# Optimization experiments

Hardware: AMD Instinct MI355X
Metric: run time of the kernel (lower is better)

## Reference

```python
import jax, jax.numpy as jnp
import numpy as np

N, E = 50000, 640000          # nodes, edges
F_IN, HID, CLS = 128, 128, 64  # feature dims


def setup_inputs() -> dict:
    key = jax.random.key(0)
    ks = jax.random.split(key, 12)
    x = jax.random.normal(ks[0], (N, F_IN), dtype=jnp.float32)
    edge_index = jax.random.randint(ks[1], (2, E), 0, N, dtype=jnp.int32)
    s_in = 1.0 / np.sqrt(F_IN)
    s_h = 1.0 / np.sqrt(HID)
    return {
        "x": x,
        "edge_index": edge_index,
        "W0": jax.random.normal(ks[2], (F_IN, HID), jnp.float32) * s_in,
        "b0": jnp.zeros((HID,), jnp.float32),
        "W1": jax.random.normal(ks[3], (HID, HID), jnp.float32) * s_h,
        "b1": jnp.zeros((HID,), jnp.float32),
        "W2": jax.random.normal(ks[4], (HID, HID), jnp.float32) * s_h,
        "b2": jnp.zeros((HID,), jnp.float32),
        "W_lin": jax.random.normal(ks[5], (HID, CLS), jnp.float32) * s_h,
        "b_lin": jnp.zeros((CLS,), jnp.float32),
    }


def reference(x, edge_index, W0, b0, W1, b1, W2, b2, W_lin, b_lin):
    # GCNConv (PyG defaults): out = D^-1/2 (A + I) D^-1/2 (x @ W) + b
    row, col = edge_index[0], edge_index[1]  # source -> target
    # degree with self-loop (graph is fixed across layers, compute norms once)
    deg = jnp.zeros((N,), x.dtype).at[col].add(1.0) + 1.0
    dinv = jax.lax.rsqrt(deg)                 # deg >= 1, safe
    enorm = (dinv[row] * dinv[col])[:, None]  # [E,1] edge norm
    snorm = (dinv * dinv)[:, None]            # [N,1] self-loop norm

    def conv(h, W, b):
        h = h @ W                                             # [N,HID]
        agg = jnp.zeros_like(h).at[col].add(h[row] * enorm)   # neighbor agg
        return agg + h * snorm + b                            # + self loop + bias

    h = jax.nn.relu(conv(x, W0, b0))
    h = jax.nn.relu(conv(h, W1, b1))
    h = jax.nn.relu(conv(h, W2, b2))
    return h @ W_lin + b_lin
```

## Files before the change

### kernel.cpp

```cpp
#include <hip/hip_runtime.h>
#include <hip/hip_fp16.h>

#define N_NODES 50000
#define HID 128
#define CLS 64

#define NBINS 196
#define NBLK 256
#define LBUF_CAP 4096
#define WTOT 57344
#define GEMM0_BLOCKS 782
#define AROW 136

typedef __attribute__((ext_vector_type(8))) _Float16 f16x8;
typedef __attribute__((ext_vector_type(4))) float f32x4;

__global__ __launch_bounds__(256) void hist_wsplit_kernel(
    const int* __restrict__ col, int* __restrict__ hist,
    const float* __restrict__ W0, const float* __restrict__ W1,
    const float* __restrict__ W2, const float* __restrict__ Wl,
    __half* __restrict__ o0h, __half* __restrict__ o0l,
    __half* __restrict__ o1h, __half* __restrict__ o1l,
    __half* __restrict__ o2h, __half* __restrict__ o2l,
    __half* __restrict__ o3h, __half* __restrict__ o3l,
    int E, int chunk) {
    int widx = blockIdx.x * 256 + threadIdx.x;
    if (widx < WTOT) {
        const float* W;
        __half *oh, *ol;
        int NCdim, local;
        if (widx < 16384)      { W = W0; oh = o0h; ol = o0l; NCdim = 128; local = widx; }
        else if (widx < 32768) { W = W1; oh = o1h; ol = o1l; NCdim = 128; local = widx - 16384; }
        else if (widx < 49152) { W = W2; oh = o2h; ol = o2l; NCdim = 128; local = widx - 32768; }
        else                   { W = Wl; oh = o3h; ol = o3l; NCdim = 64;  local = widx - 49152; }
        int nn = local >> 7;
        int k = local & 127;
        float v = W[(size_t)k * NCdim + nn];
        __half h = __float2half_rn(v);
        oh[local] = h;
        ol[local] = __float2half_rn(v - __half2float(h));
    }
    __shared__ int h[NBINS];
    for (int i = threadIdx.x; i < NBINS; i += 256) h[i] = 0;
    __syncthreads();
    int b = blockIdx.x;
    int beg = b * chunk;
    int end = min(E, beg + chunk);
    if (beg < end) {
        int vend = beg + ((end - beg) & ~3);
        for (int i = beg + threadIdx.x * 4; i < vend; i += 1024) {
            int4 c4 = *(const int4*)(col + i);
            atomicAdd(&h[c4.x >> 8], 1);
            atomicAdd(&h[c4.y >> 8], 1);
            atomicAdd(&h[c4.z >> 8], 1);
            atomicAdd(&h[c4.w >> 8], 1);
        }
        int i = vend + threadIdx.x;
        if (i < end) atomicAdd(&h[col[i] >> 8], 1);
    }
    __syncthreads();
    for (int i = threadIdx.x; i < NBINS; i += 256)
        hist[i * NBLK + b] = h[i];
}

__global__ __launch_bounds__(256) void scatter_kernel(
    const int* __restrict__ row, const int* __restrict__ col,
    const int* __restrict__ hist, int* __restrict__ binBase_g,
    int* __restrict__ sbuf_src, unsigned char* __restrict__ sbuf_c,
    int E, int chunk) {
    __shared__ int sTot[256];
    __shared__ int cur[NBINS];
    int b = blockIdx.x, t = threadIdx.x;
    int partial = 0, total = 0;
    if (t < NBINS) {
        const int4* r4 = (const int4*)(hist + t * NBLK);
        int nb4 = b >> 2, rem = b & 3;
        for (int j = 0; j < NBLK / 4; ++j) {
            int4 v = r4[j];
            int s = v.x + v.y + v.z + v.w;
            total += s;
            if (j < nb4) partial += s;
            else if (j == nb4) {
                if (rem > 0) partial += v.x;
                if (rem > 1) partial += v.y;
                if (rem > 2) partial += v.z;
            }
        }
    }
    sTot[t] = (t < NBINS) ? total : 0;
    __syncthreads();
#pragma unroll
    for (int off = 1; off < 256; off <<= 1) {
        int u = (t >= off) ? sTot[t - off] : 0;
        __syncthreads();
        sTot[t] += u;
        __syncthreads();
    }
    int myBase = sTot[t] - total;
    if (t < NBINS) cur[t] = myBase + partial;
    if (b == 0) {
        if (t < NBINS) binBase_g[t] = myBase;
        if (t == 0) binBase_g[NBINS] = E;
    }
    __syncthreads();
    int beg = b * chunk;
    int end = min(E, beg + chunk);
    if (beg >= end) return;
    int vend = beg + ((end - beg) & ~3);
    for (int i = beg + t * 4; i < vend; i += 1024) {
        int4 c4 = *(const int4*)(col + i);
        int4 r4 = *(const int4*)(row + i);
        int p;
        p = atomicAdd(&cur[c4.x >> 8], 1); sbuf_src[p] = r4.x; sbuf_c[p] = (unsigned char)(c4.x & 255);
        p = atomicAdd(&cur[c4.y >> 8], 1); sbuf_src[p] = r4.y; sbuf_c[p] = (unsigned char)(c4.y & 255);
        p = atomicAdd(&cur[c4.z >> 8], 1); sbuf_src[p] = r4.z; sbuf_c[p] = (unsigned char)(c4.z & 255);
        p = atomicAdd(&cur[c4.w >> 8], 1); sbuf_src[p] = r4.w; sbuf_c[p] = (unsigned char)(c4.w & 255);
    }
    int i = vend + t;
    if (i < end) {
        int c = col[i];
        int p = atomicAdd(&cur[c >> 8], 1);
        sbuf_src[p] = row[i];
        sbuf_c[p] = (unsigned char)(c & 255);
    }
}

__device__ __forceinline__ void gemm0_body(
    const float* __restrict__ x, const __half* __restrict__ Bh,
    const __half* __restrict__ Bl, __half* __restrict__ C, int M, int rowTile) {
    constexpr int NT = 8;
    int lane = threadIdx.x & 63;
    int m0 = rowTile << 4;
    if (m0 >= M) return;
    int mr = lane & 15;
    int kq = (lane >> 4) << 3;

    const float*  af = x + (size_t)(m0 + mr) * 128 + kq;
    const __half* bh = Bh + (size_t)mr * 128 + kq;
    const __half* bl = Bl + (size_t)mr * 128 + kq;

    f32x4 acc[NT];
#pragma unroll
    for (int t = 0; t < NT; ++t) acc[t] = (f32x4){0.f, 0.f, 0.f, 0.f};
#pragma unroll
    for (int kc = 0; kc < 128; kc += 32) {
        float4 lo = *(const float4*)(af + kc);
        float4 hi = *(const float4*)(af + kc + 4);
        f16x8 a;
        a[0] = (_Float16)lo.x; a[1] = (_Float16)lo.y;
        a[2] = (_Float16)lo.z; a[3] = (_Float16)lo.w;
        a[4] = (_Float16)hi.x; a[5] = (_Float16)hi.y;
        a[6] = (_Float16)hi.z; a[7] = (_Float16)hi.w;
#pragma unroll
        for (int t = 0; t < NT; ++t) {
            f16x8 wh = *(const f16x8*)(bh + (size_t)t * 16 * 128 + kc);
            f16x8 wl = *(const f16x8*)(bl + (size_t)t * 16 * 128 + kc);
            acc[t] = __builtin_amdgcn_mfma_f32_16x16x32_f16(a, wh, acc[t], 0, 0, 0);
            acc[t] = __builtin_amdgcn_mfma_f32_16x16x32_f16(a, wl, acc[t], 0, 0, 0);
        }
    }
    int r0 = m0 + ((lane >> 4) << 2);
    int cc = lane & 15;
#pragma unroll
    for (int t = 0; t < NT; ++t)
#pragma unroll
        for (int r = 0; r < 4; ++r)
            C[(size_t)(r0 + r) * 128 + t * 16 + cc] =
                __float2half_rn(acc[t][r]);
}

__global__ __launch_bounds__(256) void csrplace_gemm0_kernel(
    const int* __restrict__ binBase,
    const int* __restrict__ sbuf_src, const unsigned char* __restrict__ sbuf_c,
    float* __restrict__ dinv, int* __restrict__ row_ptr, int* __restrict__ csr_src,
    const float* __restrict__ x, const __half* __restrict__ W0h,
    const __half* __restrict__ W0l, __half* __restrict__ h2, int n, int E) {
    __shared__ int lcnt[256];
    __shared__ int lcur[256];
    __shared__ int ss[256];
    __shared__ int lbuf[LBUF_CAP];
    int b = blockIdx.x;
    if (b >= NBINS) {
        gemm0_body(x, W0h, W0l, h2, n, (b - NBINS) * 4 + (threadIdx.x >> 6));
        return;
    }
    int t = threadIdx.x;
    lcnt[t] = 0;
    __syncthreads();
    int beg = binBase[b], end = binBase[b + 1];
    for (int j = beg + t; j < end; j += 256)
        atomicAdd(&lcnt[sbuf_c[j]], 1);
    __syncthreads();
    int deg = lcnt[t];
    int node = b * 256 + t;
    if (node < n) dinv[node] = rsqrtf((float)deg + 1.0f);
    ss[t] = deg;
    __syncthreads();
#pragma unroll
    for (int off = 1; off < 256; off <<= 1) {
        int u = (t >= off) ? ss[t - off] : 0;
        __syncthreads();
        ss[t] += u;
        __syncthreads();
    }
    int excl = ss[t] - deg;
    lcur[t] = excl;
    int total = ss[255];
    if (node < n) row_ptr[node] = beg + excl;
    if (b == 0 && t == 0) row_ptr[n] = E;
    __syncthreads();
    for (int j = beg + t; j < end; j += 256) {
        int c = sbuf_c[j];
        int pos = atomicAdd(&lcur[c], 1);
        lbuf[pos] = sbuf_src[j];
    }
    __syncthreads();
    for (int j = t; j < total; j += 256) csr_src[beg + j] = lbuf[j];
}

template<int NC, bool HEAD>
__global__ __launch_bounds__(256) void agg_gemm_kernel(
    const __half* __restrict__ h2, const int* __restrict__ row_ptr,
    const int* __restrict__ csr_src, const float* __restrict__ dinv,
    const float* __restrict__ bias,
    const __half* __restrict__ Bh, const __half* __restrict__ Bl,
    const float* __restrict__ gbias, void* __restrict__ Cv, int n) {
    __shared__ __half Als[16][AROW];
    int wave = threadIdx.x >> 6;
    int lane = threadIdx.x & 63;
    int loff = lane << 1;
    int m0 = blockIdx.x << 4;

#pragma unroll
    for (int k = 0; k < 4; ++k) {
        int lr = wave * 4 + k;
        int wid = m0 + lr;
        if (wid >= n) break;
        int beg = row_ptr[wid];
        int end = row_ptr[wid + 1];
        float dv = dinv[wid];
        float ax = 0.f, ay = 0.f;
        for (int base = beg; base < end; base += 64) {
            int cnt = end - base;
            if (cnt > 64) cnt = 64;
            int msrc = 0;
            float mw = 0.f;
            if (lane < cnt) {
                msrc = csr_src[base + lane];
                mw = dinv[msrc] * dv;
            }
            int j = 0;
            for (; j + 8 <= cnt; j += 8) {
                int s0 = __shfl(msrc, j),     s1 = __shfl(msrc, j + 1);
                int s2 = __shfl(msrc, j + 2), s3 = __shfl(msrc, j + 3);
                int s4 = __shfl(msrc, j + 4), s5 = __shfl(msrc, j + 5);
                int s6 = __shfl(msrc, j + 6), s7 = __shfl(msrc, j + 7);
                float w0 = __shfl(mw, j),     w1 = __shfl(mw, j + 1);
                float w2 = __shfl(mw, j + 2), w3 = __shfl(mw, j + 3);
                float w4 = __shfl(mw, j + 4), w5 = __shfl(mw, j + 5);
                float w6 = __shfl(mw, j + 6), w7 = __shfl(mw, j + 7);
                float2 v0 = __half22float2(*(const __half2*)(h2 + ((size_t)s0 << 7) + loff));
                float2 v1 = __half22float2(*(const __half2*)(h2 + ((size_t)s1 << 7) + loff));
                float2 v2 = __half22float2(*(const __half2*)(h2 + ((size_t)s2 << 7) + loff));
                float2 v3 = __half22float2(*(const __half2*)(h2 + ((size_t)s3 << 7) + loff));
                float2 v4 = __half22float2(*(const __half2*)(h2 + ((size_t)s4 << 7) + loff));
                float2 v5 = __half22float2(*(const __half2*)(h2 + ((size_t)s5 << 7) + loff));
                float2 v6 = __half22float2(*(const __half2*)(h2 + ((size_t)s6 << 7) + loff));
                float2 v7 = __half22float2(*(const __half2*)(h2 + ((size_t)s7 << 7) + loff));
                ax = fmaf(v0.x, w0, ax); ay = fmaf(v0.y, w0, ay);
                ax = fmaf(v1.x, w1, ax); ay = fmaf(v1.y, w1, ay);
                ax = fmaf(v2.x, w2, ax); ay = fmaf(v2.y, w2, ay);
                ax = fmaf(v3.x, w3, ax); ay = fmaf(v3.y, w3, ay);
                ax = fmaf(v4.x, w4, ax); ay = fmaf(v4.y, w4, ay);
                ax = fmaf(v5.x, w5, ax); ay = fmaf(v5.y, w5, ay);
                ax = fmaf(v6.x, w6, ax); ay = fmaf(v6.y, w6, ay);
                ax = fmaf(v7.x, w7, ax); ay = fmaf(v7.y, w7, ay);
            }
            for (; j + 4 <= cnt; j += 4) {
                int s0 = __shfl(msrc, j),     s1 = __shfl(msrc, j + 1);
                int s2 = __shfl(msrc, j + 2), s3 = __shfl(msrc, j + 3);
                float w0 = __shfl(mw, j),     w1 = __shfl(mw, j + 1);
                float w2 = __shfl(mw, j + 2), w3 = __shfl(mw, j + 3);
                float2 v0 = __half22float2(*(const __half2*)(h2 + ((size_t)s0 << 7) + loff));
                float2 v1 = __half22float2(*(const __half2*)(h2 + ((size_t)s1 << 7) + loff));
                float2 v2 = __half22float2(*(const __half2*)(h2 + ((size_t)s2 << 7) + loff));
                float2 v3 = __half22float2(*(const __half2*)(h2 + ((size_t)s3 << 7) + loff));
                ax = fmaf(v0.x, w0, ax); ay = fmaf(v0.y, w0, ay);
                ax = fmaf(v1.x, w1, ax); ay = fmaf(v1.y, w1, ay);
                ax = fmaf(v2.x, w2, ax); ay = fmaf(v2.y, w2, ay);
                ax = fmaf(v3.x, w3, ax); ay = fmaf(v3.y, w3, ay);
            }
            for (; j < cnt; ++j) {
                int s = __shfl(msrc, j);
                float w = __shfl(mw, j);
                float2 v = __half22float2(*(const __half2*)(h2 + ((size_t)s << 7) + loff));
                ax = fmaf(v.x, w, ax); ay = fmaf(v.y, w, ay);
            }
        }
        float sn = dv * dv;
        float2 self = __half22float2(*(const __half2*)(h2 + ((size_t)wid << 7) + loff));
        float2 b = *(const float2*)(bias + loff);
        float ox = fmaxf(fmaf(self.x, sn, ax) + b.x, 0.f);
        float oy = fmaxf(fmaf(self.y, sn, ay) + b.y, 0.f);
        *(__half2*)&Als[lr][loff] = __float22half2_rn(make_float2(ox, oy));
    }
    __syncthreads();

    constexpr int NT = NC / 16;
    constexpr int TPW = NT / 4;
    int mr = lane & 15;
    int kq = (lane >> 4) << 3;
    const __half* bh = Bh + (size_t)mr * 128 + kq;
    const __half* bl = Bl + (size_t)mr * 128 + kq;

    f32x4 acc[TPW];
#pragma unroll
    for (int t = 0; t < TPW; ++t) acc[t] = (f32x4){0.f, 0.f, 0.f, 0.f};
#pragma unroll
    for (int kc = 0; kc < 128; kc += 32) {
        f16x8 a = *(const f16x8*)&Als[mr][kq + kc];
#pragma unroll
        for (int t = 0; t < TPW; ++t) {
            int tile = wave * TPW + t;
            f16x8 wh = *(const f16x8*)(bh + (size_t)tile * 16 * 128 + kc);
            f16x8 wl = *(const f16x8*)(bl + (size_t)tile * 16 * 128 + kc);
            acc[t] = __builtin_amdgcn_mfma_f32_16x16x32_f16(a, wh, acc[t], 0, 0, 0);
            acc[t] = __builtin_amdgcn_mfma_f32_16x16x32_f16(a, wl, acc[t], 0, 0, 0);
        }
    }
    int r0 = m0 + ((lane >> 4) << 2);
    int cc = lane & 15;
#pragma unroll
    for (int t = 0; t < TPW; ++t) {
        int tile = wave * TPW + t;
        float bsv = HEAD ? gbias[tile * 16 + cc] : 0.f;
#pragma unroll
        for (int r = 0; r < 4; ++r) {
            if (r0 + r >= n) break;
            size_t idx = (size_t)(r0 + r) * NC + tile * 16 + cc;
            float val = acc[t][r] + bsv;
            if (HEAD)
                ((float*)Cv)[idx] = val;
            else
                ((__half*)Cv)[idx] = __float2half_rn(val);
        }
    }
}

extern "C" void kernel_launch(void* const* d_in, const int* in_sizes, int n_in,
                              void* d_out, int out_size, void* d_ws, size_t ws_size,
                              hipStream_t stream) {
    const float* x  = (const float*)d_in[0];
    const int* ei   = (const int*)d_in[1];
    const float* W0 = (const float*)d_in[2];
    const float* b0 = (const float*)d_in[3];
    const float* W1 = (const float*)d_in[4];
    const float* b1 = (const float*)d_in[5];
    const float* W2 = (const float*)d_in[6];
    const float* b2 = (const float*)d_in[7];
    const float* Wl = (const float*)d_in[8];
    const float* bl = (const float*)d_in[9];
    float* out = (float*)d_out;

    const int N = N_NODES;
    const int E = in_sizes[1] / 2;
    const int* row = ei;
    const int* col = ei + E;
    const int chunk = (((E + NBLK - 1) / NBLK) + 3) & ~3;

    char* ws = (char*)d_ws;
    auto alloc = [&](size_t bytes) {
        char* p = ws;
        ws += (bytes + 255) & ~(size_t)255;
        return p;
    };
    int*   hist    = (int*)alloc((size_t)NBINS * NBLK * 4);
    int*   binBase = (int*)alloc((size_t)(NBINS + 1) * 4);
    int*   sbuf_src= (int*)alloc((size_t)E * 4);
    unsigned char* sbuf_c = (unsigned char*)alloc((size_t)E);
    int*   row_ptr = (int*)alloc((size_t)(N + 1) * 4);
    float* dinv    = (float*)alloc((size_t)N * 4);
    int*   csr_src = (int*)alloc((size_t)E * 4);
    __half* h2a    = (__half*)alloc((size_t)N * HID * 2);
    __half* h2b    = (__half*)alloc((size_t)N * HID * 2);
    __half* Wt_h[4];
    __half* Wt_l[4];
    for (int i = 0; i < 3; ++i) {
        Wt_h[i] = (__half*)alloc((size_t)HID * HID * 2);
        Wt_l[i] = (__half*)alloc((size_t)HID * HID * 2);
    }
    Wt_h[3] = (__half*)alloc((size_t)CLS * HID * 2);
    Wt_l[3] = (__half*)alloc((size_t)CLS * HID * 2);

    hist_wsplit_kernel<<<NBLK, 256, 0, stream>>>(col, hist, W0, W1, W2, Wl,
        Wt_h[0], Wt_l[0], Wt_h[1], Wt_l[1], Wt_h[2], Wt_l[2], Wt_h[3], Wt_l[3], E, chunk);
    scatter_kernel<<<NBLK, 256, 0, stream>>>(row, col, hist, binBase, sbuf_src, sbuf_c, E, chunk);
    csrplace_gemm0_kernel<<<NBINS + GEMM0_BLOCKS, 256, 0, stream>>>(
        binBase, sbuf_src, sbuf_c, dinv, row_ptr, csr_src,
        x, Wt_h[0], Wt_l[0], h2a, N, E);

    const int fusedBlocks = (N + 15) / 16;

    agg_gemm_kernel<128, false><<<fusedBlocks, 256, 0, stream>>>(
        h2a, row_ptr, csr_src, dinv, b0, Wt_h[1], Wt_l[1], nullptr, h2b, N);
    agg_gemm_kernel<128, false><<<fusedBlocks, 256, 0, stream>>>(
        h2b, row_ptr, csr_src, dinv, b1, Wt_h[2], Wt_l[2], nullptr, h2a, N);
    agg_gemm_kernel<64, true><<<fusedBlocks, 256, 0, stream>>>(
        h2a, row_ptr, csr_src, dinv, b2, Wt_h[3], Wt_l[3], bl, out, N);
}
```

Measured before the change: 281.0 us.

## Split neighbor gather across half-waves with wider loads and prefetched CSR rows

The aggregation now gives each half-wave alternate edges. Each lane loads 4 fp16 features (8 bytes) instead of 2, and the two halves are combined with a cross-lane xor shuffle at the end. Row pointers, the first 64 source indices and edge weights for all four rows of a wave are fetched up front, so their latencies overlap instead of being serialized per row. The goal is more gathers in flight and fewer load instructions per edge. In exchange it adds shuffle reductions and drops the per-row bounds check, which assumes the node count is a multiple of 16.

```diff
diff --git a/kernel.cpp b/kernel.cpp
--- a/kernel.cpp
+++ b/kernel.cpp
@@ -14,6 +14,17 @@
 
 typedef __attribute__((ext_vector_type(8))) _Float16 f16x8;
 typedef __attribute__((ext_vector_type(4))) float f32x4;
+
+__device__ __forceinline__ float2 u2f2(unsigned int u) {
+    union { unsigned int u; __half2 h; } c;
+    c.u = u;
+    return __half22float2(c.h);
+}
+__device__ __forceinline__ unsigned int f2u2(float a, float b) {
+    union { unsigned int u; __half2 h; } c;
+    c.h = __float22half2_rn(make_float2(a, b));
+    return c.u;
+}
 
 __global__ __launch_bounds__(256) void hist_wsplit_kernel(
     const int* __restrict__ col, int* __restrict__ hist,
@@ -218,6 +229,46 @@
     for (int j = t; j < total; j += 256) csr_src[beg + j] = lbuf[j];
 }
 
+__device__ __forceinline__ void gather_batch(
+    const __half* __restrict__ h2, int msrc, float mw, int cnt,
+    int hw, int foff, float4& acc) {
+    int pairs = (cnt + 1) >> 1;
+    int j = 0;
+    for (; j + 4 <= pairs; j += 4) {
+        int i0 = (j << 1) + hw,       i1 = ((j + 1) << 1) + hw;
+        int i2 = ((j + 2) << 1) + hw, i3 = ((j + 3) << 1) + hw;
+        int s0 = __shfl(msrc, i0), s1 = __shfl(msrc, i1);
+        int s2 = __shfl(msrc, i2), s3 = __shfl(msrc, i3);
+        float w0 = __shfl(mw, i0), w1 = __shfl(mw, i1);
+        float w2 = __shfl(mw, i2), w3 = __shfl(mw, i3);
+        uint2 r0 = *(const uint2*)(h2 + ((size_t)s0 << 7) + foff);
+        uint2 r1 = *(const uint2*)(h2 + ((size_t)s1 << 7) + foff);
+        uint2 r2 = *(const uint2*)(h2 + ((size_t)s2 << 7) + foff);
+        uint2 r3 = *(const uint2*)(h2 + ((size_t)s3 << 7) + foff);
+        float2 a0 = u2f2(r0.x), b0 = u2f2(r0.y);
+        float2 a1 = u2f2(r1.x), b1 = u2f2(r1.y);
+        float2 a2 = u2f2(r2.x), b2 = u2f2(r2.y);
+        float2 a3 = u2f2(r3.x), b3 = u2f2(r3.y);
+        acc.x = fmaf(a0.x, w0, acc.x); acc.y = fmaf(a0.y, w0, acc.y);
+        acc.z = fmaf(b0.x, w0, acc.z); acc.w = fmaf(b0.y, w0, acc.w);
+        acc.x = fmaf(a1.x, w1, acc.x); acc.y = fmaf(a1.y, w1, acc.y);
+        acc.z = fmaf(b1.x, w1, acc.z); acc.w = fmaf(b1.y, w1, acc.w);
+        acc.x = fmaf(a2.x, w2, acc.x); acc.y = fmaf(a2.y, w2, acc.y);
+        acc.z = fmaf(b2.x, w2, acc.z); acc.w = fmaf(b2.y, w2, acc.w);
+        acc.x = fmaf(a3.x, w3, acc.x); acc.y = fmaf(a3.y, w3, acc.y);
+        acc.z = fmaf(b3.x, w3, acc.z); acc.w = fmaf(b3.y, w3, acc.w);
+    }
+    for (; j < pairs; ++j) {
+        int i0 = (j << 1) + hw;
+        int s0 = __shfl(msrc, i0);
+        float w0 = __shfl(mw, i0);
+        uint2 r0 = *(const uint2*)(h2 + ((size_t)s0 << 7) + foff);
+        float2 a0 = u2f2(r0.x), b0 = u2f2(r0.y);
+        acc.x = fmaf(a0.x, w0, acc.x); acc.y = fmaf(a0.y, w0, acc.y);
+        acc.z = fmaf(b0.x, w0, acc.z); acc.w = fmaf(b0.y, w0, acc.w);
+    }
+}
+
 template<int NC, bool HEAD>
 __global__ __launch_bounds__(256) void agg_gemm_kernel(
     const __half* __restrict__ h2, const int* __restrict__ row_ptr,
@@ -225,84 +276,70 @@
     const float* __restrict__ bias,
     const __half* __restrict__ Bh, const __half* __restrict__ Bl,
     const float* __restrict__ gbias, void* __restrict__ Cv, int n) {
-    __shared__ __half Als[16][AROW];
+    __shared__ __align__(16) __half Als[16][AROW];
     int wave = threadIdx.x >> 6;
     int lane = threadIdx.x & 63;
-    int loff = lane << 1;
+    int hw = lane >> 5;
+    int foff = (lane & 31) << 2;
     int m0 = blockIdx.x << 4;
-
+    int wid_base = m0 + wave * 4;
+
+    int beg4[4], end4[4];
+    float dv4[4];
 #pragma unroll
     for (int k = 0; k < 4; ++k) {
-        int lr = wave * 4 + k;
-        int wid = m0 + lr;
-        if (wid >= n) break;
-        int beg = row_ptr[wid];
-        int end = row_ptr[wid + 1];
-        float dv = dinv[wid];
-        float ax = 0.f, ay = 0.f;
-        for (int base = beg; base < end; base += 64) {
-            int cnt = end - base;
-            if (cnt > 64) cnt = 64;
+        beg4[k] = row_ptr[wid_base + k];
+        end4[k] = row_ptr[wid_base + k + 1];
+        dv4[k] = dinv[wid_base + k];
+    }
+    int msrc4[4];
+#pragma unroll
+    for (int k = 0; k < 4; ++k) {
+        int cnt = min(64, end4[k] - beg4[k]);
+        msrc4[k] = 0;
+        if (lane < cnt) msrc4[k] = csr_src[beg4[k] + lane];
+    }
+    float mw4[4];
+#pragma unroll
+    for (int k = 0; k < 4; ++k) {
+        int cnt = min(64, end4[k] - beg4[k]);
+        mw4[k] = 0.f;
+        if (lane < cnt) mw4[k] = dinv[msrc4[k]] * dv4[k];
+    }
+
+#pragma unroll
+    for (int k = 0; k < 4; ++k) {
+        int wid = wid_base + k;
+        float dv = dv4[k];
+        float4 acc = make_float4(0.f, 0.f, 0.f, 0.f);
+        int cnt0 = min(64, end4[k] - beg4[k]);
+        gather_batch(h2, msrc4[k], mw4[k], cnt0, hw, foff, acc);
+        for (int base = beg4[k] + 64; base < end4[k]; base += 64) {
+            int cnt = min(64, end4[k] - base);
             int msrc = 0;
             float mw = 0.f;
             if (lane < cnt) {
                 msrc = csr_src[base + lane];
                 mw = dinv[msrc] * dv;
             }
-            int j = 0;
-            for (; j + 8 <= cnt; j += 8) {
-                int s0 = __shfl(msrc, j),     s1 = __shfl(msrc, j + 1);
-                int s2 = __shfl(msrc, j + 2), s3 = __shfl(msrc, j + 3);
-                int s4 = __shfl(msrc, j + 4), s5 = __shfl(msrc, j + 5);
-                int s6 = __shfl(msrc, j + 6), s7 = __shfl(msrc, j + 7);
-                float w0 = __shfl(mw, j),     w1 = __shfl(mw, j + 1);
-                float w2 = __shfl(mw, j + 2), w3 = __shfl(mw, j + 3);
-                float w4 = __shfl(mw, j + 4), w5 = __shfl(mw, j + 5);
-                float w6 = __shfl(mw, j + 6), w7 = __shfl(mw, j + 7);
-                float2 v0 = __half22float2(*(const __half2*)(h2 + ((size_t)s0 << 7) + loff));
-                float2 v1 = __half22float2(*(const __half2*)(h2 + ((size_t)s1 << 7) + loff));
-                float2 v2 = __half22float2(*(const __half2*)(h2 + ((size_t)s2 << 7) + loff));
-                float2 v3 = __half22float2(*(const __half2*)(h2 + ((size_t)s3 << 7) + loff));
-                float2 v4 = __half22float2(*(const __half2*)(h2 + ((size_t)s4 << 7) + loff));
-                float2 v5 = __half22float2(*(const __half2*)(h2 + ((size_t)s5 << 7) + loff));
-                float2 v6 = __half22float2(*(const __half2*)(h2 + ((size_t)s6 << 7) + loff));
-                float2 v7 = __half22float2(*(const __half2*)(h2 + ((size_t)s7 << 7) + loff));
-                ax = fmaf(v0.x, w0, ax); ay = fmaf(v0.y, w0, ay);
-                ax = fmaf(v1.x, w1, ax); ay = fmaf(v1.y, w1, ay);
-                ax = fmaf(v2.x, w2, ax); ay = fmaf(v2.y, w2, ay);
-                ax = fmaf(v3.x, w3, ax); ay = fmaf(v3.y, w3, ay);
-                ax = fmaf(v4.x, w4, ax); ay = fmaf(v4.y, w4, ay);
-                ax = fmaf(v5.x, w5, ax); ay = fmaf(v5.y, w5, ay);
-                ax = fmaf(v6.x, w6, ax); ay = fmaf(v6.y, w6, ay);
-                ax = fmaf(v7.x, w7, ax); ay = fmaf(v7.y, w7, ay);
-            }
-            for (; j + 4 <= cnt; j += 4) {
-                int s0 = __shfl(msrc, j),     s1 = __shfl(msrc, j + 1);
-                int s2 = __shfl(msrc, j + 2), s3 = __shfl(msrc, j + 3);
-                float w0 = __shfl(mw, j),     w1 = __shfl(mw, j + 1);
-                float w2 = __shfl(mw, j + 2), w3 = __shfl(mw, j + 3);
-                float2 v0 = __half22float2(*(const __half2*)(h2 + ((size_t)s0 << 7) + loff));
-                float2 v1 = __half22float2(*(const __half2*)(h2 + ((size_t)s1 << 7) + loff));
-                float2 v2 = __half22float2(*(const __half2*)(h2 + ((size_t)s2 << 7) + loff));
-                float2 v3 = __half22float2(*(const __half2*)(h2 + ((size_t)s3 << 7) + loff));
-                ax = fmaf(v0.x, w0, ax); ay = fmaf(v0.y, w0, ay);
-                ax = fmaf(v1.x, w1, ax); ay = fmaf(v1.y, w1, ay);
-                ax = fmaf(v2.x, w2, ax); ay = fmaf(v2.y, w2, ay);
-                ax = fmaf(v3.x, w3, ax); ay = fmaf(v3.y, w3, ay);
-            }
-            for (; j < cnt; ++j) {
-                int s = __shfl(msrc, j);
-                float w = __shfl(mw, j);
-                float2 v = __half22float2(*(const __half2*)(h2 + ((size_t)s << 7) + loff));
-                ax = fmaf(v.x, w, ax); ay = fmaf(v.y, w, ay);
-            }
-        }
+            gather_batch(h2, msrc, mw, cnt, hw, foff, acc);
+        }
+        acc.x += __shfl_xor(acc.x, 32);
+        acc.y += __shfl_xor(acc.y, 32);
+        acc.z += __shfl_xor(acc.z, 32);
+        acc.w += __shfl_xor(acc.w, 32);
         float sn = dv * dv;
-        float2 self = __half22float2(*(const __half2*)(h2 + ((size_t)wid << 7) + loff));
-        float2 b = *(const float2*)(bias + loff);
-        float ox = fmaxf(fmaf(self.x, sn, ax) + b.x, 0.f);
-        float oy = fmaxf(fmaf(self.y, sn, ay) + b.y, 0.f);
-        *(__half2*)&Als[lr][loff] = __float22half2_rn(make_float2(ox, oy));
+        uint2 sr = *(const uint2*)(h2 + ((size_t)wid << 7) + foff);
+        float2 s01 = u2f2(sr.x), s23 = u2f2(sr.y);
+        float4 b4 = *(const float4*)(bias + foff);
+        float o0 = fmaxf(fmaf(s01.x, sn, acc.x) + b4.x, 0.f);
+        float o1 = fmaxf(fmaf(s01.y, sn, acc.y) + b4.y, 0.f);
+        float o2 = fmaxf(fmaf(s23.x, sn, acc.z) + b4.z, 0.f);
+        float o3 = fmaxf(fmaf(s23.y, sn, acc.w) + b4.w, 0.f);
+        if (hw == 0) {
+            int lr = wave * 4 + k;
+            *(uint2*)&Als[lr][foff] = make_uint2(f2u2(o0, o1), f2u2(o2, o3));
+        }
     }
     __syncthreads();
 
```

Result: slower. 287.5 us (+2.3%).
